# Performance work log

Measured on AMD Instinct MI355X. Metric: run time of the kernel, lower is better.

Reference implementation:

```python
import jax, jax.numpy as jnp
import numpy as np

N_HEADS = 8
N_NODES = 100_000
DEG = 16
N_EDGES = N_NODES * DEG
IN_DIM = 256
OUT_DIM = 128


def setup_inputs() -> dict:
    key = jax.random.key(0)
    k1, k2, k3, k4 = jax.random.split(key, 4)
    X = jax.random.normal(k1, (N_NODES, IN_DIM), dtype=jnp.float32)
    weights = jax.random.normal(k2, (IN_DIM, OUT_DIM), dtype=jnp.float32) * (1.0 / np.sqrt(IN_DIM))
    attention_w = jax.random.normal(k3, (1, N_HEADS), dtype=jnp.float32) * 0.1
    # valid CSR with uniform degree DEG
    row_pointers = (jnp.arange(N_NODES + 1, dtype=jnp.int32) * DEG)
    column_index = jax.random.randint(k4, (N_EDGES,), 0, N_NODES, dtype=jnp.int32)
    # TC-GNN block bookkeeping tensors: kernel-schedule metadata, no effect on math
    blockPartition = jnp.zeros(((N_NODES + 15) // 16,), dtype=jnp.int32)
    edgeToColumn = jnp.zeros((N_EDGES,), dtype=jnp.int32)
    edgeToRow = jnp.zeros((N_EDGES,), dtype=jnp.int32)
    return {
        "X": X,
        "weights": weights,
        "attention_w": attention_w,
        "row_pointers": row_pointers,
        "column_index": column_index,
        "blockPartition": blockPartition,
        "edgeToColumn": edgeToColumn,
        "edgeToRow": edgeToRow,
    }


def reference(X, weights, attention_w, row_pointers, column_index,
              blockPartition, edgeToColumn, edgeToRow):
    n_nodes = X.shape[0]
    n_edges = column_index.shape[0]
    # dense projection: X_prime = X @ W  -> [n_nodes, out_dim]
    X_prime = X @ weights
    # CSR row id of each edge: row_ids[e] = r s.t. row_pointers[r] <= e < row_pointers[r+1]
    row_ids = jnp.searchsorted(row_pointers,
                               jnp.arange(n_edges, dtype=row_pointers.dtype),
                               side="right") - 1
    # SDDMM (GAcc.forward_ef): per-edge scalar feature = <X_prime[src], X_prime[dst]>
    dst = X_prime[column_index]                    # [E, out_dim]
    edge_feature = jnp.sum(X_prime[row_ids] * dst, axis=-1)  # [E]
    # edge_attentions = outer(edge_feature, attention_w) -> [n_heads, E];
    # aggregation kernel collapses heads: att_e = edge_feature_e * sum_h(w_h)
    att = edge_feature * jnp.sum(attention_w)      # [E]
    # attention-weighted SpMM (GAcc.forward_gat): scatter-add into destination rows
    out = jax.ops.segment_sum(att[:, None] * dst, row_ids, num_segments=n_nodes)
    return out
```

## Files before the change

### kernel.cpp

```cpp
#include <hip/hip_runtime.h>
#include <hip/hip_bf16.h>
#include <stdint.h>

#define N_NODES 100000
#define IN_DIM 256
#define OUT_DIM 128
#define DEG 16

typedef __bf16 bf16x8 __attribute__((ext_vector_type(8)));
typedef __bf16 bf16x4 __attribute__((ext_vector_type(4)));
typedef float f32x4 __attribute__((ext_vector_type(4)));

__global__ void prep_w_kernel(const float* __restrict__ W, __bf16* __restrict__ Wt) {
    const int j = blockIdx.x;
    const int k = threadIdx.x;
    Wt[j * IN_DIM + k] = (__bf16)W[k * OUT_DIM + j];
}

__global__ __launch_bounds__(256) void gemm_kernel(const float* __restrict__ X,
                                                   const __bf16* __restrict__ Wt,
                                                   __bf16* __restrict__ XP) {
    __shared__ __bf16 Alds[64][264];
    const int t = threadIdx.x;
    const int m0 = blockIdx.x * 64;

    #pragma unroll
    for (int i = 0; i < 16; ++i) {
        const int flat = i * 256 + t;
        const int row  = flat >> 6;
        const int col  = (flat & 63) * 4;
        int grow = m0 + row;
        if (grow >= N_NODES) grow = N_NODES - 1;
        float4 v = *reinterpret_cast<const float4*>(X + (size_t)grow * IN_DIM + col);
        bf16x4 b;
        b[0] = (__bf16)v.x; b[1] = (__bf16)v.y; b[2] = (__bf16)v.z; b[3] = (__bf16)v.w;
        *reinterpret_cast<bf16x4*>(&Alds[row][col]) = b;
    }
    __syncthreads();

    const int lane = t & 63;
    const int wave = t >> 6;
    const int n0 = wave * 32;
    const int lr = lane & 15;
    const int lg = lane >> 4;

    f32x4 acc[4][2] = {};
    const __bf16* bp0 = Wt + (size_t)(n0 + lr) * IN_DIM + lg * 8;
    const __bf16* bp1 = bp0 + 16 * IN_DIM;

    #pragma unroll
    for (int ks = 0; ks < 8; ++ks) {
        const int ko = ks * 32 + lg * 8;
        bf16x8 b0 = *reinterpret_cast<const bf16x8*>(bp0 + ks * 32);
        bf16x8 b1 = *reinterpret_cast<const bf16x8*>(bp1 + ks * 32);
        bf16x8 a[4];
        #pragma unroll
        for (int mi = 0; mi < 4; ++mi)
            a[mi] = *reinterpret_cast<const bf16x8*>(&Alds[mi * 16 + lr][ko]);
        #pragma unroll
        for (int mi = 0; mi < 4; ++mi) {
            acc[mi][0] = __builtin_amdgcn_mfma_f32_16x16x32_bf16(a[mi], b0, acc[mi][0], 0, 0, 0);
            acc[mi][1] = __builtin_amdgcn_mfma_f32_16x16x32_bf16(a[mi], b1, acc[mi][1], 0, 0, 0);
        }
    }

    #pragma unroll
    for (int mi = 0; mi < 4; ++mi)
        #pragma unroll
        for (int ni = 0; ni < 2; ++ni)
            #pragma unroll
            for (int r = 0; r < 4; ++r) {
                const int row = m0 + mi * 16 + lg * 4 + r;
                if (row < N_NODES) {
                    const int col = n0 + ni * 16 + lr;
                    XP[(size_t)row * OUT_DIM + col] = (__bf16)acc[mi][ni][r];
                }
            }
}

__global__ __launch_bounds__(256) void gat_edge_kernel(const __bf16* __restrict__ XP,
                                                       const int* __restrict__ rp,
                                                       const int* __restrict__ ci,
                                                       const float* __restrict__ attw,
                                                       float* __restrict__ out) {
    const int lane = threadIdx.x & 63;
    const int row = blockIdx.x * 4 + (threadIdx.x >> 6);
    const int g = lane >> 4;
    const int sl = lane & 15;

    float s = 0.f;
    #pragma unroll
    for (int h = 0; h < 8; ++h) s += attw[h];

    float x[8];
    {
        uint4 xv = *reinterpret_cast<const uint4*>(XP + (size_t)row * OUT_DIM + sl * 8);
        const uint32_t* xw = reinterpret_cast<const uint32_t*>(&xv);
        #pragma unroll
        for (int i = 0; i < 4; ++i) {
            x[2 * i]     = __uint_as_float(xw[i] << 16);
            x[2 * i + 1] = __uint_as_float(xw[i] & 0xffff0000u);
        }
    }

    const int4 cv = reinterpret_cast<const int4*>(ci + (size_t)row * DEG)[g];
    const int c[4] = {cv.x, cv.y, cv.z, cv.w};

    uint4 dvu[4];
    #pragma unroll
    for (int j = 0; j < 4; ++j)
        dvu[j] = *reinterpret_cast<const uint4*>(XP + (size_t)c[j] * OUT_DIM + sl * 8);

    float d[4][8];
    #pragma unroll
    for (int j = 0; j < 4; ++j) {
        const uint32_t* dw = reinterpret_cast<const uint32_t*>(&dvu[j]);
        #pragma unroll
        for (int i = 0; i < 4; ++i) {
            d[j][2 * i]     = __uint_as_float(dw[i] << 16);
            d[j][2 * i + 1] = __uint_as_float(dw[i] & 0xffff0000u);
        }
    }

    float p[4];
    #pragma unroll
    for (int j = 0; j < 4; ++j) {
        float t0 = 0.f;
        #pragma unroll
        for (int i = 0; i < 8; ++i) t0 += x[i] * d[j][i];
        p[j] = t0;
    }
    #pragma unroll
    for (int off = 1; off <= 8; off <<= 1) {
        #pragma unroll
        for (int j = 0; j < 4; ++j) p[j] += __shfl_xor(p[j], off);
    }

    float acc[8] = {};
    #pragma unroll
    for (int j = 0; j < 4; ++j) {
        const float att = p[j] * s;
        #pragma unroll
        for (int i = 0; i < 8; ++i) acc[i] += att * d[j][i];
    }

    #pragma unroll
    for (int off = 16; off <= 32; off <<= 1) {
        #pragma unroll
        for (int i = 0; i < 8; ++i) acc[i] += __shfl_xor(acc[i], off);
    }

    if (g == 0) {
        float4 o0, o1;
        o0.x = acc[0]; o0.y = acc[1]; o0.z = acc[2]; o0.w = acc[3];
        o1.x = acc[4]; o1.y = acc[5]; o1.z = acc[6]; o1.w = acc[7];
        float* dst = out + (size_t)row * OUT_DIM + sl * 8;
        *reinterpret_cast<float4*>(dst) = o0;
        *reinterpret_cast<float4*>(dst + 4) = o1;
    }
}

extern "C" void kernel_launch(void* const* d_in, const int* in_sizes, int n_in,
                              void* d_out, int out_size, void* d_ws, size_t ws_size,
                              hipStream_t stream) {
    const float* X    = (const float*)d_in[0];
    const float* W    = (const float*)d_in[1];
    const float* attw = (const float*)d_in[2];
    const int*   rp   = (const int*)d_in[3];
    const int*   ci   = (const int*)d_in[4];
    float* out = (float*)d_out;

    __bf16* XP = (__bf16*)d_ws;
    __bf16* Wt = (__bf16*)((char*)d_ws + (size_t)N_NODES * OUT_DIM * 2);

    prep_w_kernel<<<OUT_DIM, IN_DIM, 0, stream>>>(W, Wt);
    gemm_kernel<<<(N_NODES + 63) / 64, 256, 0, stream>>>(X, Wt, XP);
    gat_edge_kernel<<<N_NODES / 4, 256, 0, stream>>>(XP, rp, ci, attw, out);
}
```

Before: 97.42 us.

## Restructure GAT edge kernel mapping, split GEMM staging into halves, coalesce W prep

The edge kernel now gives each 16-lane group a whole row and processes all 16 neighbours per group. This removes the cross-group shuffle reduction and the idle lanes at the store, and issues 16 gathers per lane in flight, using packed float2 math. The GEMM stages X into LDS in two K-halves so the second half's global loads overlap the first half's MFMAs. The weight transpose kernel now reads coalesced. The cost is much higher register pressure in the edge kernel (16 uint4 held at once), which may lower occupancy.

After: 96.87 us. Within noise of the previous version (-0.6%).

```diff
diff --git a/kernel.cpp b/kernel.cpp
--- a/kernel.cpp
+++ b/kernel.cpp
@@ -10,33 +10,21 @@
 typedef __bf16 bf16x8 __attribute__((ext_vector_type(8)));
 typedef __bf16 bf16x4 __attribute__((ext_vector_type(4)));
 typedef float f32x4 __attribute__((ext_vector_type(4)));
+typedef float f32x2 __attribute__((ext_vector_type(2)));
 
 __global__ void prep_w_kernel(const float* __restrict__ W, __bf16* __restrict__ Wt) {
-    const int j = blockIdx.x;
-    const int k = threadIdx.x;
-    Wt[j * IN_DIM + k] = (__bf16)W[k * OUT_DIM + j];
+    const int idx = blockIdx.x * 256 + threadIdx.x;
+    const int k = idx >> 7;
+    const int j = idx & 127;
+    Wt[j * IN_DIM + k] = (__bf16)W[idx];
 }
 
 __global__ __launch_bounds__(256) void gemm_kernel(const float* __restrict__ X,
                                                    const __bf16* __restrict__ Wt,
                                                    __bf16* __restrict__ XP) {
-    __shared__ __bf16 Alds[64][264];
+    __shared__ __bf16 Alds[2][64][136];
     const int t = threadIdx.x;
     const int m0 = blockIdx.x * 64;
-
-    #pragma unroll
-    for (int i = 0; i < 16; ++i) {
-        const int flat = i * 256 + t;
-        const int row  = flat >> 6;
-        const int col  = (flat & 63) * 4;
-        int grow = m0 + row;
-        if (grow >= N_NODES) grow = N_NODES - 1;
-        float4 v = *reinterpret_cast<const float4*>(X + (size_t)grow * IN_DIM + col);
-        bf16x4 b;
-        b[0] = (__bf16)v.x; b[1] = (__bf16)v.y; b[2] = (__bf16)v.z; b[3] = (__bf16)v.w;
-        *reinterpret_cast<bf16x4*>(&Alds[row][col]) = b;
-    }
-    __syncthreads();
 
     const int lane = t & 63;
     const int wave = t >> 6;
@@ -44,25 +32,50 @@
     const int lr = lane & 15;
     const int lg = lane >> 4;
 
+    const int scol = (t & 31) * 4;
+
+    auto stage = [&](int h) {
+        #pragma unroll
+        for (int i = 0; i < 8; ++i) {
+            const int row = i * 8 + (t >> 5);
+            int grow = m0 + row;
+            if (grow >= N_NODES) grow = N_NODES - 1;
+            float4 v = *reinterpret_cast<const float4*>(
+                X + (size_t)grow * IN_DIM + h * 128 + scol);
+            bf16x4 b;
+            b[0] = (__bf16)v.x; b[1] = (__bf16)v.y; b[2] = (__bf16)v.z; b[3] = (__bf16)v.w;
+            *reinterpret_cast<bf16x4*>(&Alds[h][row][scol]) = b;
+        }
+    };
+
     f32x4 acc[4][2] = {};
     const __bf16* bp0 = Wt + (size_t)(n0 + lr) * IN_DIM + lg * 8;
     const __bf16* bp1 = bp0 + 16 * IN_DIM;
 
-    #pragma unroll
-    for (int ks = 0; ks < 8; ++ks) {
-        const int ko = ks * 32 + lg * 8;
-        bf16x8 b0 = *reinterpret_cast<const bf16x8*>(bp0 + ks * 32);
-        bf16x8 b1 = *reinterpret_cast<const bf16x8*>(bp1 + ks * 32);
-        bf16x8 a[4];
+    auto compute_half = [&](int h) {
         #pragma unroll
-        for (int mi = 0; mi < 4; ++mi)
-            a[mi] = *reinterpret_cast<const bf16x8*>(&Alds[mi * 16 + lr][ko]);
-        #pragma unroll
-        for (int mi = 0; mi < 4; ++mi) {
-            acc[mi][0] = __builtin_amdgcn_mfma_f32_16x16x32_bf16(a[mi], b0, acc[mi][0], 0, 0, 0);
-            acc[mi][1] = __builtin_amdgcn_mfma_f32_16x16x32_bf16(a[mi], b1, acc[mi][1], 0, 0, 0);
+        for (int ks = 0; ks < 4; ++ks) {
+            const int ko = ks * 32 + lg * 8;
+            bf16x8 b0 = *reinterpret_cast<const bf16x8*>(bp0 + h * 128 + ks * 32);
+            bf16x8 b1 = *reinterpret_cast<const bf16x8*>(bp1 + h * 128 + ks * 32);
+            bf16x8 a[4];
+            #pragma unroll
+            for (int mi = 0; mi < 4; ++mi)
+                a[mi] = *reinterpret_cast<const bf16x8*>(&Alds[h][mi * 16 + lr][ko]);
+            #pragma unroll
+            for (int mi = 0; mi < 4; ++mi) {
+                acc[mi][0] = __builtin_amdgcn_mfma_f32_16x16x32_bf16(a[mi], b0, acc[mi][0], 0, 0, 0);
+                acc[mi][1] = __builtin_amdgcn_mfma_f32_16x16x32_bf16(a[mi], b1, acc[mi][1], 0, 0, 0);
+            }
         }
-    }
+    };
+
+    stage(0);
+    __syncthreads();
+    stage(1);
+    compute_half(0);
+    __syncthreads();
+    compute_half(1);
 
     #pragma unroll
     for (int mi = 0; mi < 4; ++mi)
@@ -84,80 +97,78 @@
                                                        const float* __restrict__ attw,
                                                        float* __restrict__ out) {
     const int lane = threadIdx.x & 63;
-    const int row = blockIdx.x * 4 + (threadIdx.x >> 6);
+    const int wave = threadIdx.x >> 6;
     const int g = lane >> 4;
     const int sl = lane & 15;
+    const int row = blockIdx.x * 16 + wave * 4 + g;
 
     float s = 0.f;
     #pragma unroll
     for (int h = 0; h < 8; ++h) s += attw[h];
 
-    float x[8];
+    const uint4 xv = *reinterpret_cast<const uint4*>(XP + (size_t)row * OUT_DIM + sl * 8);
+    f32x2 x2[4];
     {
-        uint4 xv = *reinterpret_cast<const uint4*>(XP + (size_t)row * OUT_DIM + sl * 8);
         const uint32_t* xw = reinterpret_cast<const uint32_t*>(&xv);
         #pragma unroll
         for (int i = 0; i < 4; ++i) {
-            x[2 * i]     = __uint_as_float(xw[i] << 16);
-            x[2 * i + 1] = __uint_as_float(xw[i] & 0xffff0000u);
+            x2[i].x = __uint_as_float(xw[i] << 16);
+            x2[i].y = __uint_as_float(xw[i] & 0xffff0000u);
         }
     }
 
-    const int4 cv = reinterpret_cast<const int4*>(ci + (size_t)row * DEG)[g];
-    const int c[4] = {cv.x, cv.y, cv.z, cv.w};
+    const int4* cb = reinterpret_cast<const int4*>(ci + (size_t)row * DEG);
+    const int4 i0 = cb[0], i1 = cb[1], i2 = cb[2], i3 = cb[3];
+    const int c[16] = {i0.x, i0.y, i0.z, i0.w, i1.x, i1.y, i1.z, i1.w,
+                       i2.x, i2.y, i2.z, i2.w, i3.x, i3.y, i3.z, i3.w};
 
-    uint4 dvu[4];
+    uint4 dv[16];
     #pragma unroll
-    for (int j = 0; j < 4; ++j)
-        dvu[j] = *reinterpret_cast<const uint4*>(XP + (size_t)c[j] * OUT_DIM + sl * 8);
+    for (int j = 0; j < 16; ++j)
+        dv[j] = *reinterpret_cast<const uint4*>(XP + (size_t)c[j] * OUT_DIM + sl * 8);
 
-    float d[4][8];
+    f32x2 acc2[4] = {};
+
     #pragma unroll
-    for (int j = 0; j < 4; ++j) {
-        const uint32_t* dw = reinterpret_cast<const uint32_t*>(&dvu[j]);
+    for (int jb = 0; jb < 4; ++jb) {
+        f32x2 d2[4][4];
         #pragma unroll
-        for (int i = 0; i < 4; ++i) {
-            d[j][2 * i]     = __uint_as_float(dw[i] << 16);
-            d[j][2 * i + 1] = __uint_as_float(dw[i] & 0xffff0000u);
+        for (int j = 0; j < 4; ++j) {
+            const uint32_t* dw = reinterpret_cast<const uint32_t*>(&dv[jb * 4 + j]);
+            #pragma unroll
+            for (int i = 0; i < 4; ++i) {
+                d2[j][i].x = __uint_as_float(dw[i] << 16);
+                d2[j][i].y = __uint_as_float(dw[i] & 0xffff0000u);
+            }
+        }
+        float p[4];
+        #pragma unroll
+        for (int j = 0; j < 4; ++j) {
+            f32x2 t = x2[0] * d2[j][0];
+            #pragma unroll
+            for (int i = 1; i < 4; ++i) t += x2[i] * d2[j][i];
+            p[j] = t.x + t.y;
+        }
+        #pragma unroll
+        for (int off = 1; off <= 8; off <<= 1) {
+            #pragma unroll
+            for (int j = 0; j < 4; ++j) p[j] += __shfl_xor(p[j], off);
+        }
+        #pragma unroll
+        for (int j = 0; j < 4; ++j) {
+            const float att = p[j] * s;
+            f32x2 a2; a2.x = att; a2.y = att;
+            #pragma unroll
+            for (int i = 0; i < 4; ++i) acc2[i] += a2 * d2[j][i];
         }
     }
 
-    float p[4];
-    #pragma unroll
-    for (int j = 0; j < 4; ++j) {
-        float t0 = 0.f;
-        #pragma unroll
-        for (int i = 0; i < 8; ++i) t0 += x[i] * d[j][i];
-        p[j] = t0;
-    }
-    #pragma unroll
-    for (int off = 1; off <= 8; off <<= 1) {
-        #pragma unroll
-        for (int j = 0; j < 4; ++j) p[j] += __shfl_xor(p[j], off);
-    }
-
-    float acc[8] = {};
-    #pragma unroll
-    for (int j = 0; j < 4; ++j) {
-        const float att = p[j] * s;
-        #pragma unroll
-        for (int i = 0; i < 8; ++i) acc[i] += att * d[j][i];
-    }
-
-    #pragma unroll
-    for (int off = 16; off <= 32; off <<= 1) {
-        #pragma unroll
-        for (int i = 0; i < 8; ++i) acc[i] += __shfl_xor(acc[i], off);
-    }
-
-    if (g == 0) {
-        float4 o0, o1;
-        o0.x = acc[0]; o0.y = acc[1]; o0.z = acc[2]; o0.w = acc[3];
-        o1.x = acc[4]; o1.y = acc[5]; o1.z = acc[6]; o1.w = acc[7];
-        float* dst = out + (size_t)row * OUT_DIM + sl * 8;
-        *reinterpret_cast<float4*>(dst) = o0;
-        *reinterpret_cast<float4*>(dst + 4) = o1;
-    }
+    float4 o0, o1;
+    o0.x = acc2[0].x; o0.y = acc2[0].y; o0.z = acc2[1].x; o0.w = acc2[1].y;
+    o1.x = acc2[2].x; o1.y = acc2[2].y; o1.z = acc2[3].x; o1.w = acc2[3].y;
+    float* dst = out + (size_t)row * OUT_DIM + sl * 8;
+    *reinterpret_cast<float4*>(dst) = o0;
+    *reinterpret_cast<float4*>(dst + 4) = o1;
 }
 
 extern "C" void kernel_launch(void* const* d_in, const int* in_sizes, int n_in,
@@ -173,7 +184,7 @@
     __bf16* XP = (__bf16*)d_ws;
     __bf16* Wt = (__bf16*)((char*)d_ws + (size_t)N_NODES * OUT_DIM * 2);
 
-    prep_w_kernel<<<OUT_DIM, IN_DIM, 0, stream>>>(W, Wt);
+    prep_w_kernel<<<(IN_DIM * OUT_DIM) / 256, 256, 0, stream>>>(W, Wt);
     gemm_kernel<<<(N_NODES + 63) / 64, 256, 0, stream>>>(X, Wt, XP);
-    gat_edge_kernel<<<N_NODES / 4, 256, 0, stream>>>(XP, rp, ci, attw, out);
+    gat_edge_kernel<<<N_NODES / 16, 256, 0, stream>>>(XP, rp, ci, attw, out);
 }
```
